# Kernel optimization log

Measured on AMD Instinct MI355X. Metric: run time of the kernel, lower is better.

The kernel has to match this reference:

```python
import jax, jax.numpy as jnp
import numpy as np

B, T, S, D, H, F = 8, 1024, 1024, 512, 8, 2048
LN_EPS = 1e-5


def _layernorm(x, g, b):
    m = jnp.mean(x, axis=-1, keepdims=True)
    v = jnp.mean((x - m) ** 2, axis=-1, keepdims=True)
    return (x - m) / jnp.sqrt(v + LN_EPS) * g + b


def setup_inputs() -> dict:
    key = jax.random.key(0)
    ks = jax.random.split(key, 32)
    p = lambda k, shape: jax.random.normal(k, shape, jnp.float32) * 0.02
    causal = jnp.where(jnp.triu(jnp.ones((T, T), dtype=bool), 1), -1e9, 0.0).astype(jnp.float32)
    return {
        "x": jax.random.normal(ks[0], (B, T, D), jnp.float32),
        "src_padding_mask": jnp.zeros((B, S, 1), jnp.float32),
        "src_subsq_mask": jnp.zeros((S, S), jnp.float32),  # unused by DecoderLayer math
        "tgt_padding_mask": jnp.zeros((B, T, 1), jnp.float32),
        "tgt_subsq_mask": causal,
        "mem_keys": jax.random.normal(ks[1], (B, S, D), jnp.float32),
        "mem_values": jax.random.normal(ks[2], (B, S, D), jnp.float32),
        # self-attention per-head params, stacked over heads (each head is full-D)
        "Wq_self": p(ks[3], (H, D, D)), "bq_self": p(ks[4], (H, D)),
        "Wk_self": p(ks[5], (H, D, D)), "bk_self": p(ks[6], (H, D)),
        "Wv_self": p(ks[7], (H, D, D)), "bv_self": p(ks[8], (H, D)),
        "Wo_self": p(ks[9], (H * D, D)), "bo_self": p(ks[10], (D,)),
        # memory (cross) attention: only Q per head; keys/values come from encoder
        "Wq_mem": p(ks[11], (H, D, D)), "bq_mem": p(ks[12], (H, D)),
        "Wo_mem": p(ks[13], (H * D, D)), "bo_mem": p(ks[14], (D,)),
        # FFN
        "W1": p(ks[15], (D, F)), "b1": p(ks[16], (F,)),
        "W2": p(ks[17], (F, D)), "b2": p(ks[18], (D,)),
        # LayerNorms
        "ln1_g": jnp.ones((D,), jnp.float32), "ln1_b": jnp.zeros((D,), jnp.float32),
        "ln2_g": jnp.ones((D,), jnp.float32), "ln2_b": jnp.zeros((D,), jnp.float32),
        "ln3_g": jnp.ones((D,), jnp.float32), "ln3_b": jnp.zeros((D,), jnp.float32),
    }


def reference(x, src_padding_mask, src_subsq_mask, tgt_padding_mask, tgt_subsq_mask,
              mem_keys, mem_values,
              Wq_self, bq_self, Wk_self, bk_self, Wv_self, bv_self, Wo_self, bo_self,
              Wq_mem, bq_mem, Wo_mem, bo_mem,
              W1, b1, W2, b2,
              ln1_g, ln1_b, ln2_g, ln2_b, ln3_g, ln3_b):
    b, t, d = x.shape
    h = Wq_self.shape[0]
    inv_sqrt_d = 1.0 / (d ** 0.5)

    # ---- multi-head self-attention (each head full d_model) ----
    q = jnp.einsum('btd,hde->bhte', x, Wq_self) + bq_self[None, :, None, :]
    k = jnp.einsum('btd,hde->bhte', x, Wk_self) + bk_self[None, :, None, :]
    v = jnp.einsum('btd,hde->bhte', x, Wv_self) + bv_self[None, :, None, :]
    att = jnp.einsum('bhte,bhse->bhts', q, k) * inv_sqrt_d
    att = att + tgt_padding_mask.transpose(0, 2, 1)[:, None, :, :]  # [B,1,1,T]
    att = att + tgt_subsq_mask[None, None, :, :]                     # [1,1,T,T]
    a = jax.nn.softmax(att, axis=-1)
    ho = jnp.einsum('bhts,bhse->bhte', a, v)
    cat = ho.transpose(0, 2, 1, 3).reshape(b, t, h * d)  # matches torch.cat head order
    sa = cat @ Wo_self + bo_self
    x1 = _layernorm(sa + x, ln1_g, ln1_b)  # dropout is identity at eval

    # ---- multi-head memory (cross) attention; keys/values shared across heads ----
    qm = jnp.einsum('btd,hde->bhte', x1, Wq_mem) + bq_mem[None, :, None, :]
    attm = jnp.einsum('bhte,bse->bhts', qm, mem_keys) * inv_sqrt_d
    attm = attm + src_padding_mask.transpose(0, 2, 1)[:, None, :, :]
    am = jax.nn.softmax(attm, axis=-1)
    hom = jnp.einsum('bhts,bse->bhte', am, mem_values)
    catm = hom.transpose(0, 2, 1, 3).reshape(b, t, h * d)
    ma = catm @ Wo_mem + bo_mem
    x2 = _layernorm(ma + x1, ln2_g, ln2_b)

    # ---- FFN ----
    ff = jax.nn.relu(x2 @ W1 + b1) @ W2 + b2
    out = _layernorm(ff + x2, ln3_g, ln3_b)
    return out
```

## Files before the change

### kernel.cpp

```cpp
#include <hip/hip_runtime.h>
#include <hip/hip_bf16.h>
#include <cstdint>

#define DEV __device__ __forceinline__

typedef __bf16 bf16_t;
typedef bf16_t bf16x8 __attribute__((ext_vector_type(8)));
typedef float  f32x4  __attribute__((ext_vector_type(4)));

static constexpr int B_ = 8, T_ = 1024, S_ = 1024, D_ = 512, H_ = 8, F_ = 2048;

typedef const __attribute__((address_space(1))) void* gas_ptr;
typedef __attribute__((address_space(3))) void* las_ptr;

DEV void gload_lds16(const void* g, void* l) {
  __builtin_amdgcn_global_load_lds((gas_ptr)g, (las_ptr)l, 16, 0, 0);
}

template<typename OutT, int EPI, int MI>
__global__ __launch_bounds__(256, (MI == 2) ? 3 : 2) void gemm_bt(
    const bf16_t* __restrict__ A,  int64_t aH, int64_t aB, int lda,
    const bf16_t* __restrict__ BT, int64_t bH, int64_t bB, int ldb,
    OutT* __restrict__ C,          int64_t cH, int64_t cB, int ldo,
    int K, int ZB,
    const float* __restrict__ bias, int64_t biasH, int64_t biasB,
    float scale,
    const float* __restrict__ pad, int64_t padB,
    const float* __restrict__ subsq, int subsq_ld, int causal,
    int initC, int kcap)
{
  constexpr int BM = MI * 32;

  const unsigned gx = gridDim.x, gy = gridDim.y;
  const unsigned nwg = gx * gy * gridDim.z;
  const unsigned orig = (blockIdx.z * gy + blockIdx.y) * gx + blockIdx.x;
  const unsigned q8 = nwg >> 3, r8 = nwg & 7;
  const unsigned xcd = orig & 7, cidx = orig >> 3;
  const unsigned swz = (xcd < r8 ? xcd * (q8 + 1)
                                 : r8 * (q8 + 1) + (xcd - r8) * q8) + cidx;
  const unsigned bz = swz / (gx * gy);
  const unsigned rm = swz - bz * gx * gy;
  const unsigned by = rm / gx;
  const unsigned bx = rm - by * gx;

  const int z  = bz;
  const int zh = z / ZB, zb = z - zh * ZB;
  A  += zh * aH + zb * aB;
  BT += zh * bH + zb * bB;
  C  += zh * cH + zb * cB;
  const int m0 = by * BM;
  const int n0 = bx << 7;

  __shared__ __align__(16) bf16_t As[2][BM * 64];
  __shared__ __align__(16) bf16_t Bs[2][128 * 64];

  const int tid  = threadIdx.x;
  const int lane = tid & 63;
  const int wr   = tid >> 7;
  const int wc   = (tid >> 6) & 1;

  f32x4 acc[MI][4] = {};

  const bool skip = (EPI == 2) && causal && (n0 >= m0 + BM);

  int Klim = K;
  if (kcap) { const int lim = m0 + BM; Klim = lim < K ? lim : K; }

  auto stage = [&](int buf, int kb) {
    #pragma unroll
    for (int i = 0; i < MI; ++i) {
      const int c = i * 256 + tid;
      const int row = c >> 3;
      const int col = (((c & 7) ^ (row & 7)) << 3);
      gload_lds16(A + (int64_t)(m0 + row) * lda + kb + col, &As[buf][c * 8]);
    }
    #pragma unroll
    for (int i = 0; i < 4; ++i) {
      const int c = i * 256 + tid;
      const int row = c >> 3;
      const int col = (((c & 7) ^ (row & 7)) << 3);
      gload_lds16(BT + (int64_t)(n0 + row) * ldb + kb + col, &Bs[buf][c * 8]);
    }
  };

  if (!skip) {
    const int NT = Klim >> 6;
    stage(0, 0);
    if (NT > 1) stage(1, 64);
    const int hi = lane >> 4, r7 = lane & 7;
    for (int t = 0; t < NT; ++t) {
      if (t + 1 < NT) {
        if constexpr (MI == 2) asm volatile("s_waitcnt vmcnt(6)" ::: "memory");
        else                   asm volatile("s_waitcnt vmcnt(8)" ::: "memory");
      } else {
        asm volatile("s_waitcnt vmcnt(0)" ::: "memory");
      }
      __builtin_amdgcn_s_barrier();
      __builtin_amdgcn_sched_barrier(0);
      const int cur = t & 1;
      bf16x8 af[MI][2], bq[4][2];
      #pragma unroll
      for (int ks = 0; ks < 2; ++ks) {
        #pragma unroll
        for (int i = 0; i < MI; ++i)
          af[i][ks] = *(const bf16x8*)&As[cur][(wr * (MI * 16) + i * 16 + (lane & 15)) * 64 + (((ks * 4 + hi) ^ r7) << 3)];
        #pragma unroll
        for (int i = 0; i < 4; ++i)
          bq[i][ks] = *(const bf16x8*)&Bs[cur][(wc * 64 + i * 16 + (lane & 15)) * 64 + (((ks * 4 + hi) ^ r7) << 3)];
      }
      asm volatile("s_waitcnt lgkmcnt(0)" ::: "memory");
      __builtin_amdgcn_sched_barrier(0);
      __builtin_amdgcn_s_barrier();
      if (t + 2 < NT) stage(cur, (t + 2) << 6);
      __builtin_amdgcn_sched_barrier(0);
      __builtin_amdgcn_s_setprio(1);
      #pragma unroll
      for (int ks = 0; ks < 2; ++ks)
        #pragma unroll
        for (int mi = 0; mi < MI; ++mi)
          #pragma unroll
          for (int ni = 0; ni < 4; ++ni)
            acc[mi][ni] = __builtin_amdgcn_mfma_f32_16x16x32_bf16(af[mi][ks], bq[ni][ks], acc[mi][ni], 0, 0, 0);
      __builtin_amdgcn_s_setprio(0);
    }
  }

  const float* bz_ = (EPI != 2 && bias) ? bias + zh * biasH + zb * biasB : nullptr;
  const float* pz  = (EPI == 2 && pad)  ? pad + zb * padB : nullptr;
  #pragma unroll
  for (int ni = 0; ni < 4; ++ni) {
    const int col = n0 + wc * 64 + ni * 16 + (lane & 15);
    const float badd = bz_ ? bz_[col] : 0.f;
    const float pv   = pz ? pz[col] : 0.f;
    #pragma unroll
    for (int mi = 0; mi < MI; ++mi) {
      const int rowb = m0 + wr * (MI * 16) + mi * 16 + ((lane >> 4) << 2);
      #pragma unroll
      for (int r = 0; r < 4; ++r) {
        const int row = rowb + r;
        const int64_t idx = (int64_t)row * ldo + col;
        float v = acc[mi][ni][r];
        if (EPI == 2) {
          if (skip) v = -1e9f;
          else {
            v = v * scale + pv;
            if (subsq) v += subsq[(int64_t)row * subsq_ld + col];
          }
        } else if (EPI == 3) {
          v += initC ? badd : (float)C[idx];
        } else {
          v += badd;
          if (EPI == 1) v = fmaxf(v, 0.f);
        }
        if constexpr (sizeof(OutT) == 2) C[idx] = (OutT)v;
        else                             C[idx] = v;
      }
    }
  }
}

__global__ __launch_bounds__(256) void softmax1024b(bf16_t* __restrict__ P)
{
  const int64_t row = blockIdx.x;
  const int tid = threadIdx.x;
  union { bf16_t b[4]; uint2 u; } in;
  in.u = ((const uint2*)(P + row * 1024))[tid];
  const float v0 = (float)in.b[0], v1 = (float)in.b[1];
  const float v2 = (float)in.b[2], v3 = (float)in.b[3];
  float m = fmaxf(fmaxf(v0, v1), fmaxf(v2, v3));
  #pragma unroll
  for (int off = 32; off; off >>= 1) m = fmaxf(m, __shfl_xor(m, off));
  __shared__ float red[8];
  if ((tid & 63) == 0) red[tid >> 6] = m;
  __syncthreads();
  m = fmaxf(fmaxf(red[0], red[1]), fmaxf(red[2], red[3]));
  const float e0 = __expf(v0 - m), e1 = __expf(v1 - m);
  const float e2 = __expf(v2 - m), e3 = __expf(v3 - m);
  float s = e0 + e1 + e2 + e3;
  #pragma unroll
  for (int off = 32; off; off >>= 1) s += __shfl_xor(s, off);
  if ((tid & 63) == 0) red[4 + (tid >> 6)] = s;
  __syncthreads();
  const float inv = 1.f / (red[4] + red[5] + red[6] + red[7]);
  union { bf16_t b[4]; uint2 u; } o;
  o.b[0] = (bf16_t)(e0 * inv); o.b[1] = (bf16_t)(e1 * inv);
  o.b[2] = (bf16_t)(e2 * inv); o.b[3] = (bf16_t)(e3 * inv);
  ((uint2*)(P + row * 1024))[tid] = o.u;
}

__global__ __launch_bounds__(128) void add_ln512(
    const float* __restrict__ a, const float* __restrict__ r,
    const float* __restrict__ g, const float* __restrict__ be,
    float* __restrict__ yf, bf16_t* __restrict__ yb)
{
  const int64_t row = blockIdx.x;
  const int tid = threadIdx.x;
  const float4 va = ((const float4*)(a + row * 512))[tid];
  const float4 vr = ((const float4*)(r + row * 512))[tid];
  const float x0 = va.x + vr.x, x1 = va.y + vr.y, x2 = va.z + vr.z, x3 = va.w + vr.w;
  float s = x0 + x1 + x2 + x3;
  float q = x0 * x0 + x1 * x1 + x2 * x2 + x3 * x3;
  #pragma unroll
  for (int off = 32; off; off >>= 1) { s += __shfl_xor(s, off); q += __shfl_xor(q, off); }
  __shared__ float red[4];
  if ((tid & 63) == 0) { red[tid >> 6] = s; red[2 + (tid >> 6)] = q; }
  __syncthreads();
  s = red[0] + red[1]; q = red[2] + red[3];
  const float mean = s * (1.f / 512.f);
  const float var  = q * (1.f / 512.f) - mean * mean;
  const float rstd = rsqrtf(var + 1e-5f);
  const float4 g4 = ((const float4*)g)[tid];
  const float4 b4 = ((const float4*)be)[tid];
  const float y0 = (x0 - mean) * rstd * g4.x + b4.x;
  const float y1 = (x1 - mean) * rstd * g4.y + b4.y;
  const float y2 = (x2 - mean) * rstd * g4.z + b4.z;
  const float y3 = (x3 - mean) * rstd * g4.w + b4.w;
  float4 o; o.x = y0; o.y = y1; o.z = y2; o.w = y3;
  ((float4*)(yf + row * 512))[tid] = o;
  if (yb) {
    union { bf16_t b[4]; uint2 u; } ob;
    ob.b[0] = (bf16_t)y0; ob.b[1] = (bf16_t)y1; ob.b[2] = (bf16_t)y2; ob.b[3] = (bf16_t)y3;
    ((uint2*)(yb + row * 512))[tid] = ob.u;
  }
}

template<typename InT>
__global__ __launch_bounds__(256) void tcast(
    const InT* __restrict__ src, bf16_t* __restrict__ dst, int R, int C)
{
  __shared__ float t[32][33];
  const int64_t zo = (int64_t)blockIdx.z * R * C;
  const int c0 = blockIdx.x << 5, r0 = blockIdx.y << 5;
  const int tx = threadIdx.x & 31, ty = threadIdx.x >> 5;
  #pragma unroll
  for (int i = 0; i < 32; i += 8)
    t[ty + i][tx] = (float)src[zo + (int64_t)(r0 + ty + i) * C + c0 + tx];
  __syncthreads();
  #pragma unroll
  for (int i = 0; i < 32; i += 8)
    dst[zo + (int64_t)(c0 + ty + i) * R + r0 + tx] = (bf16_t)t[tx][ty + i];
}

__global__ __launch_bounds__(256) void castf2b(
    const float* __restrict__ s, bf16_t* __restrict__ d, int n4)
{
  const int i = blockIdx.x * 256 + threadIdx.x;
  if (i >= n4) return;
  const float4 v = ((const float4*)s)[i];
  union { bf16_t b[4]; uint2 u; } o;
  o.b[0] = (bf16_t)v.x; o.b[1] = (bf16_t)v.y; o.b[2] = (bf16_t)v.z; o.b[3] = (bf16_t)v.w;
  ((uint2*)d)[i] = o.u;
}

__global__ __launch_bounds__(256) void pack3(
    const float* __restrict__ a, const float* __restrict__ b,
    const float* __restrict__ c, float* __restrict__ d, int n)
{
  const int i = blockIdx.x * 256 + threadIdx.x;
  if (i < n) { d[i] = a[i]; d[n + i] = b[i]; d[2 * n + i] = c[i]; }
}

extern "C" void kernel_launch(void* const* d_in, const int* in_sizes, int n_in,
                              void* d_out, int out_size, void* d_ws, size_t ws_size,
                              hipStream_t stream)
{
  const float* x       = (const float*)d_in[0];
  const float* src_pad = (const float*)d_in[1];
  const float* tgt_pad = (const float*)d_in[3];
  const float* tgt_sub = (const float*)d_in[4];
  const float* mk      = (const float*)d_in[5];
  const float* mv      = (const float*)d_in[6];
  const float* Wq  = (const float*)d_in[7];
  const float* bq  = (const float*)d_in[8];
  const float* Wk  = (const float*)d_in[9];
  const float* bk  = (const float*)d_in[10];
  const float* Wv  = (const float*)d_in[11];
  const float* bv  = (const float*)d_in[12];
  const float* Wo  = (const float*)d_in[13];
  const float* bo  = (const float*)d_in[14];
  const float* Wqm = (const float*)d_in[15];
  const float* bqm = (const float*)d_in[16];
  const float* Wom = (const float*)d_in[17];
  const float* bom = (const float*)d_in[18];
  const float* W1  = (const float*)d_in[19];
  const float* b1  = (const float*)d_in[20];
  const float* W2  = (const float*)d_in[21];
  const float* b2  = (const float*)d_in[22];
  const float* g1  = (const float*)d_in[23];
  const float* be1 = (const float*)d_in[24];
  const float* g2  = (const float*)d_in[25];
  const float* be2 = (const float*)d_in[26];
  const float* g3  = (const float*)d_in[27];
  const float* be3 = (const float*)d_in[28];
  float* outf = (float*)d_out;

  constexpr int64_t BTD = (int64_t)B_ * T_ * D_;
  constexpr int64_t BTS = (int64_t)B_ * T_ * S_;
  constexpr int64_t DD  = (int64_t)D_ * D_;
  const int M8 = B_ * T_;

  char* p = (char*)d_ws;
  auto alloc = [&](int64_t bytes) -> void* {
    char* r = p; p += (bytes + 255) & ~(int64_t)255; return (void*)r;
  };
  bf16_t* WTqkv = (bf16_t*)alloc(3 * H_ * DD * 2);
  bf16_t* WoT   = (bf16_t*)alloc((int64_t)D_ * H_ * D_ * 2);
  bf16_t* WqmT  = (bf16_t*)alloc(H_ * DD * 2);
  bf16_t* WomT  = (bf16_t*)alloc((int64_t)D_ * H_ * D_ * 2);
  bf16_t* W1T   = (bf16_t*)alloc((int64_t)F_ * D_ * 2);
  bf16_t* W2T   = (bf16_t*)alloc((int64_t)D_ * F_ * 2);
  float*  bqkv  = (float*)alloc(3 * H_ * D_ * 4);
  bf16_t* actb  = (bf16_t*)alloc(BTD * 2);
  bf16_t* mkb   = (bf16_t*)alloc(BTD * 2);
  bf16_t* mvT   = (bf16_t*)alloc(BTD * 2);
  float*  x1f   = (float*)alloc(BTD * 4);

  const int64_t remain = (int64_t)ws_size - (int64_t)(p - (char*)d_ws);
  const int64_t perG   = 3 * BTD * 2 + BTD * 2 + BTS * 2;
  const int64_t hoCat  = (int64_t)B_ * T_ * H_ * D_ * 2;
  int G = 0;
  for (int g = 8; g >= 1; g >>= 1)
    if (remain >= hoCat + (int64_t)g * perG + (4 << 20)) { G = g; break; }
  const int64_t needB = 3 * BTD * 2 + BTD * 2 + BTS * 2 + BTD * 2 + (1 << 20);
  if (G == 0 && remain < needB) return;

  const float scale = 1.0f / sqrtf((float)D_);
  dim3 blk(256);

  castf2b<<<dim3((unsigned)(BTD / 4 / 256)), blk, 0, stream>>>(x, actb, (int)(BTD / 4));
  castf2b<<<dim3((unsigned)(BTD / 4 / 256)), blk, 0, stream>>>(mk, mkb, (int)(BTD / 4));
  tcast<float><<<dim3(D_ / 32, S_ / 32, B_), blk, 0, stream>>>(mv, mvT, S_, D_);
  tcast<float><<<dim3(D_ / 32, D_ / 32, H_), blk, 0, stream>>>(Wq, WTqkv, D_, D_);
  tcast<float><<<dim3(D_ / 32, D_ / 32, H_), blk, 0, stream>>>(Wk, WTqkv + H_ * DD, D_, D_);
  tcast<float><<<dim3(D_ / 32, D_ / 32, H_), blk, 0, stream>>>(Wv, WTqkv + 2 * H_ * DD, D_, D_);
  tcast<float><<<dim3(D_ / 32, (H_ * D_) / 32, 1), blk, 0, stream>>>(Wo, WoT, H_ * D_, D_);
  tcast<float><<<dim3(D_ / 32, D_ / 32, H_), blk, 0, stream>>>(Wqm, WqmT, D_, D_);
  tcast<float><<<dim3(D_ / 32, (H_ * D_) / 32, 1), blk, 0, stream>>>(Wom, WomT, H_ * D_, D_);
  tcast<float><<<dim3(F_ / 32, D_ / 32, 1), blk, 0, stream>>>(W1, W1T, D_, F_);
  tcast<float><<<dim3(D_ / 32, F_ / 32, 1), blk, 0, stream>>>(W2, W2T, F_, D_);
  pack3<<<dim3((H_ * D_ + 255) / 256), blk, 0, stream>>>(bq, bk, bv, bqkv, H_ * D_);

  bf16_t* ffh = nullptr;

  if (G > 0) {
    bf16_t* hoAll = (bf16_t*)alloc(hoCat);
    bf16_t* qkv   = (bf16_t*)alloc(3 * G * BTD * 2);
    bf16_t* vt    = (bf16_t*)alloc((int64_t)G * BTD * 2);
    bf16_t* logit = (bf16_t*)alloc((int64_t)G * BTS * 2);
    ffh = qkv;

    for (int h0 = 0; h0 < H_; h0 += G) {
      gemm_bt<bf16_t, 0, 4><<<dim3(D_ / 128, M8 / 128, 3 * G), blk, 0, stream>>>(
          actb, 0, 0, D_,
          WTqkv + (int64_t)h0 * DD, (int64_t)H_ * DD, DD, D_,
          qkv, (int64_t)G * BTD, BTD, D_,
          D_, G,
          bqkv + h0 * D_, (int64_t)H_ * D_, D_,
          1.f, nullptr, 0, nullptr, 0, 0, 0, 0);
      tcast<bf16_t><<<dim3(D_ / 32, T_ / 32, G * B_), blk, 0, stream>>>(
          qkv + (int64_t)2 * G * BTD, vt, T_, D_);
      gemm_bt<bf16_t, 2, 4><<<dim3(S_ / 128, T_ / 128, G * B_), blk, 0, stream>>>(
          qkv, BTD, (int64_t)T_ * D_, D_,
          qkv + (int64_t)G * BTD, BTD, (int64_t)T_ * D_, D_,
          logit, BTS, (int64_t)T_ * S_, S_,
          D_, B_,
          nullptr, 0, 0,
          scale, tgt_pad, T_, tgt_sub, S_, 1, 0, 0);
      softmax1024b<<<dim3((unsigned)(G * B_ * T_)), blk, 0, stream>>>(logit);
      gemm_bt<bf16_t, 0, 4><<<dim3(D_ / 128, T_ / 128, G * B_), blk, 0, stream>>>(
          logit, BTS, (int64_t)T_ * S_, S_,
          vt, (int64_t)B_ * D_ * T_, (int64_t)D_ * T_, T_,
          hoAll + (int64_t)h0 * D_, D_, (int64_t)T_ * H_ * D_, H_ * D_,
          S_, B_,
          nullptr, 0, 0, 1.f, nullptr, 0, nullptr, 0, 0, 0, 1);
    }
    gemm_bt<float, 0, 2><<<dim3(D_ / 128, M8 / 64, 1), blk, 0, stream>>>(
        hoAll, 0, 0, H_ * D_, WoT, 0, 0, H_ * D_, outf, 0, 0, D_,
        H_ * D_, 1, bo, 0, 0, 1.f, nullptr, 0, nullptr, 0, 0, 0, 0);
    add_ln512<<<dim3(M8), dim3(128), 0, stream>>>(outf, x, g1, be1, x1f, actb);

    for (int h0 = 0; h0 < H_; h0 += G) {
      gemm_bt<bf16_t, 0, 4><<<dim3(D_ / 128, M8 / 128, G), blk, 0, stream>>>(
          actb, 0, 0, D_,
          WqmT + (int64_t)h0 * DD, 0, DD, D_,
          qkv, 0, BTD, D_,
          D_, G,
          bqm + h0 * D_, 0, D_,
          1.f, nullptr, 0, nullptr, 0, 0, 0, 0);
      gemm_bt<bf16_t, 2, 4><<<dim3(S_ / 128, T_ / 128, G * B_), blk, 0, stream>>>(
          qkv, BTD, (int64_t)T_ * D_, D_,
          mkb, 0, (int64_t)S_ * D_, D_,
          logit, BTS, (int64_t)T_ * S_, S_,
          D_, B_,
          nullptr, 0, 0,
          scale, src_pad, S_, nullptr, 0, 0, 0, 0);
      softmax1024b<<<dim3((unsigned)(G * B_ * T_)), blk, 0, stream>>>(logit);
      gemm_bt<bf16_t, 0, 4><<<dim3(D_ / 128, T_ / 128, G * B_), blk, 0, stream>>>(
          logit, BTS, (int64_t)T_ * S_, S_,
          mvT, 0, (int64_t)D_ * S_, S_,
          hoAll + (int64_t)h0 * D_, D_, (int64_t)T_ * H_ * D_, H_ * D_,
          S_, B_,
          nullptr, 0, 0, 1.f, nullptr, 0, nullptr, 0, 0, 0, 0);
    }
    gemm_bt<float, 0, 2><<<dim3(D_ / 128, M8 / 64, 1), blk, 0, stream>>>(
        hoAll, 0, 0, H_ * D_, WomT, 0, 0, H_ * D_, outf, 0, 0, D_,
        H_ * D_, 1, bom, 0, 0, 1.f, nullptr, 0, nullptr, 0, 0, 0, 0);
    add_ln512<<<dim3(M8), dim3(128), 0, stream>>>(outf, x1f, g2, be2, x1f, actb);
  } else {
    bf16_t* qkvH  = (bf16_t*)alloc(3 * BTD * 2);
    bf16_t* vtH   = (bf16_t*)alloc(BTD * 2);
    bf16_t* logit = (bf16_t*)alloc(BTS * 2);
    bf16_t* hoH   = (bf16_t*)alloc(BTD * 2);
    ffh = qkvH;

    for (int h = 0; h < H_; ++h) {
      gemm_bt<bf16_t, 0, 4><<<dim3(D_ / 128, M8 / 128, 3), blk, 0, stream>>>(
          actb, 0, 0, D_,
          WTqkv + (int64_t)h * DD, (int64_t)H_ * DD, 0, D_,
          qkvH, BTD, 0, D_,
          D_, 1,
          bqkv + h * D_, (int64_t)H_ * D_, 0,
          1.f, nullptr, 0, nullptr, 0, 0, 0, 0);
      tcast<bf16_t><<<dim3(D_ / 32, T_ / 32, B_), blk, 0, stream>>>(
          qkvH + 2 * BTD, vtH, T_, D_);
      gemm_bt<bf16_t, 2, 4><<<dim3(S_ / 128, T_ / 128, B_), blk, 0, stream>>>(
          qkvH, 0, (int64_t)T_ * D_, D_,
          qkvH + BTD, 0, (int64_t)T_ * D_, D_,
          logit, 0, (int64_t)T_ * S_, S_,
          D_, B_,
          nullptr, 0, 0,
          scale, tgt_pad, T_, tgt_sub, S_, 1, 0, 0);
      softmax1024b<<<dim3((unsigned)(B_ * T_)), blk, 0, stream>>>(logit);
      gemm_bt<bf16_t, 0, 4><<<dim3(D_ / 128, T_ / 128, B_), blk, 0, stream>>>(
          logit, 0, (int64_t)T_ * S_, S_,
          vtH, 0, (int64_t)D_ * T_, T_,
          hoH, 0, (int64_t)T_ * D_, D_,
          S_, B_,
          nullptr, 0, 0, 1.f, nullptr, 0, nullptr, 0, 0, 0, 1);
      gemm_bt<float, 3, 2><<<dim3(D_ / 128, M8 / 64, 1), blk, 0, stream>>>(
          hoH, 0, 0, D_,
          WoT + (int64_t)h * D_, 0, 0, H_ * D_,
          outf, 0, 0, D_,
          D_, 1,
          bo, 0, 0, 1.f, nullptr, 0, nullptr, 0, 0, (h == 0) ? 1 : 0, 0);
    }
    add_ln512<<<dim3(M8), dim3(128), 0, stream>>>(outf, x, g1, be1, x1f, actb);

    for (int h = 0; h < H_; ++h) {
      gemm_bt<bf16_t, 0, 4><<<dim3(D_ / 128, M8 / 128, 1), blk, 0, stream>>>(
          actb, 0, 0, D_,
          WqmT + (int64_t)h * DD, 0, 0, D_,
          qkvH, 0, 0, D_,
          D_, 1,
          bqm + h * D_, 0, 0,
          1.f, nullptr, 0, nullptr, 0, 0, 0, 0);
      gemm_bt<bf16_t, 2, 4><<<dim3(S_ / 128, T_ / 128, B_), blk, 0, stream>>>(
          qkvH, 0, (int64_t)T_ * D_, D_,
          mkb, 0, (int64_t)S_ * D_, D_,
          logit, 0, (int64_t)T_ * S_, S_,
          D_, B_,
          nullptr, 0, 0,
          scale, src_pad, S_, nullptr, 0, 0, 0, 0);
      softmax1024b<<<dim3((unsigned)(B_ * T_)), blk, 0, stream>>>(logit);
      gemm_bt<bf16_t, 0, 4><<<dim3(D_ / 128, T_ / 128, B_), blk, 0, stream>>>(
          logit, 0, (int64_t)T_ * S_, S_,
          mvT, 0, (int64_t)D_ * S_, S_,
          hoH, 0, (int64_t)T_ * D_, D_,
          S_, B_,
          nullptr, 0, 0, 1.f, nullptr, 0, nullptr, 0, 0, 0, 0);
      gemm_bt<float, 3, 2><<<dim3(D_ / 128, M8 / 64, 1), blk, 0, stream>>>(
          hoH, 0, 0, D_,
          WomT + (int64_t)h * D_, 0, 0, H_ * D_,
          outf, 0, 0, D_,
          D_, 1,
          bom, 0, 0, 1.f, nullptr, 0, nullptr, 0, 0, (h == 0) ? 1 : 0, 0);
    }
    add_ln512<<<dim3(M8), dim3(128), 0, stream>>>(outf, x1f, g2, be2, x1f, actb);
  }

  gemm_bt<bf16_t, 1, 4><<<dim3(F_ / 128, M8 / 128, 1), blk, 0, stream>>>(
      actb, 0, 0, D_, W1T, 0, 0, D_, ffh, 0, 0, F_,
      D_, 1, b1, 0, 0, 1.f, nullptr, 0, nullptr, 0, 0, 0, 0);
  gemm_bt<float, 0, 2><<<dim3(D_ / 128, M8 / 64, 1), blk, 0, stream>>>(
      ffh, 0, 0, F_, W2T, 0, 0, F_, outf, 0, 0, D_,
      F_, 1, b2, 0, 0, 1.f, nullptr, 0, nullptr, 0, 0, 0, 0);
  add_ln512<<<dim3(M8), dim3(128), 0, stream>>>(outf, x1f, g3, be3, outf, nullptr);

  (void)in_sizes; (void)n_in; (void)out_size;
}
```

Measured before the change: 1.147 ms.

## Skip masked causal tiles and use 64-row GEMM tiles throughout

Adds a causal mode in which fully masked logit tiles return early instead of writing -1e9. The softmax is templated so the causal variant reads and exponentiates only the valid prefix of each row, and writes only up to the next 64-column boundary. The PV GEMM's K cap then keeps unwritten entries out of the product. All bf16 GEMMs also switch from 128-row to 64-row tiles, raising block count and occupancy at the cost of less operand reuse per block.

```diff
diff --git a/kernel.cpp b/kernel.cpp
--- a/kernel.cpp
+++ b/kernel.cpp
@@ -51,6 +51,9 @@
   const int m0 = by * BM;
   const int n0 = bx << 7;
 
+  const bool skip = (EPI == 2) && causal && (n0 >= m0 + BM);
+  if (skip && causal == 2) return;
+
   __shared__ __align__(16) bf16_t As[2][BM * 64];
   __shared__ __align__(16) bf16_t Bs[2][128 * 64];
 
@@ -60,8 +63,6 @@
   const int wc   = (tid >> 6) & 1;
 
   f32x4 acc[MI][4] = {};
-
-  const bool skip = (EPI == 2) && causal && (n0 >= m0 + BM);
 
   int Klim = K;
   if (kcap) { const int lim = m0 + BM; Klim = lim < K ? lim : K; }
@@ -159,14 +160,22 @@
   }
 }
 
+template<int CAUSAL>
 __global__ __launch_bounds__(256) void softmax1024b(bf16_t* __restrict__ P)
 {
   const int64_t row = blockIdx.x;
+  const int len = CAUSAL ? (int)(row % T_) + 1 : 1024;
   const int tid = threadIdx.x;
-  union { bf16_t b[4]; uint2 u; } in;
-  in.u = ((const uint2*)(P + row * 1024))[tid];
-  const float v0 = (float)in.b[0], v1 = (float)in.b[1];
-  const float v2 = (float)in.b[2], v3 = (float)in.b[3];
+  const int j4 = tid << 2;
+  float v0 = -3e38f, v1 = -3e38f, v2 = -3e38f, v3 = -3e38f;
+  if (j4 < len) {
+    union { bf16_t b[4]; uint2 u; } in;
+    in.u = ((const uint2*)(P + row * 1024))[tid];
+    v0 = (float)in.b[0];
+    if (j4 + 1 < len) v1 = (float)in.b[1];
+    if (j4 + 2 < len) v2 = (float)in.b[2];
+    if (j4 + 3 < len) v3 = (float)in.b[3];
+  }
   float m = fmaxf(fmaxf(v0, v1), fmaxf(v2, v3));
   #pragma unroll
   for (int off = 32; off; off >>= 1) m = fmaxf(m, __shfl_xor(m, off));
@@ -174,18 +183,23 @@
   if ((tid & 63) == 0) red[tid >> 6] = m;
   __syncthreads();
   m = fmaxf(fmaxf(red[0], red[1]), fmaxf(red[2], red[3]));
-  const float e0 = __expf(v0 - m), e1 = __expf(v1 - m);
-  const float e2 = __expf(v2 - m), e3 = __expf(v3 - m);
+  const float e0 = (j4     < len) ? __expf(v0 - m) : 0.f;
+  const float e1 = (j4 + 1 < len) ? __expf(v1 - m) : 0.f;
+  const float e2 = (j4 + 2 < len) ? __expf(v2 - m) : 0.f;
+  const float e3 = (j4 + 3 < len) ? __expf(v3 - m) : 0.f;
   float s = e0 + e1 + e2 + e3;
   #pragma unroll
   for (int off = 32; off; off >>= 1) s += __shfl_xor(s, off);
   if ((tid & 63) == 0) red[4 + (tid >> 6)] = s;
   __syncthreads();
   const float inv = 1.f / (red[4] + red[5] + red[6] + red[7]);
-  union { bf16_t b[4]; uint2 u; } o;
-  o.b[0] = (bf16_t)(e0 * inv); o.b[1] = (bf16_t)(e1 * inv);
-  o.b[2] = (bf16_t)(e2 * inv); o.b[3] = (bf16_t)(e3 * inv);
-  ((uint2*)(P + row * 1024))[tid] = o.u;
+  const int lenc = CAUSAL ? ((len + 63) & ~63) : 1024;
+  if (j4 < lenc) {
+    union { bf16_t b[4]; uint2 u; } o;
+    o.b[0] = (bf16_t)(e0 * inv); o.b[1] = (bf16_t)(e1 * inv);
+    o.b[2] = (bf16_t)(e2 * inv); o.b[3] = (bf16_t)(e3 * inv);
+    ((uint2*)(P + row * 1024))[tid] = o.u;
+  }
 }
 
 __global__ __launch_bounds__(128) void add_ln512(
@@ -350,7 +364,7 @@
     ffh = qkv;
 
     for (int h0 = 0; h0 < H_; h0 += G) {
-      gemm_bt<bf16_t, 0, 4><<<dim3(D_ / 128, M8 / 128, 3 * G), blk, 0, stream>>>(
+      gemm_bt<bf16_t, 0, 2><<<dim3(D_ / 128, M8 / 64, 3 * G), blk, 0, stream>>>(
           actb, 0, 0, D_,
           WTqkv + (int64_t)h0 * DD, (int64_t)H_ * DD, DD, D_,
           qkv, (int64_t)G * BTD, BTD, D_,
@@ -359,15 +373,15 @@
           1.f, nullptr, 0, nullptr, 0, 0, 0, 0);
       tcast<bf16_t><<<dim3(D_ / 32, T_ / 32, G * B_), blk, 0, stream>>>(
           qkv + (int64_t)2 * G * BTD, vt, T_, D_);
-      gemm_bt<bf16_t, 2, 4><<<dim3(S_ / 128, T_ / 128, G * B_), blk, 0, stream>>>(
+      gemm_bt<bf16_t, 2, 2><<<dim3(S_ / 128, T_ / 64, G * B_), blk, 0, stream>>>(
           qkv, BTD, (int64_t)T_ * D_, D_,
           qkv + (int64_t)G * BTD, BTD, (int64_t)T_ * D_, D_,
           logit, BTS, (int64_t)T_ * S_, S_,
           D_, B_,
           nullptr, 0, 0,
-          scale, tgt_pad, T_, tgt_sub, S_, 1, 0, 0);
-      softmax1024b<<<dim3((unsigned)(G * B_ * T_)), blk, 0, stream>>>(logit);
-      gemm_bt<bf16_t, 0, 4><<<dim3(D_ / 128, T_ / 128, G * B_), blk, 0, stream>>>(
+          scale, tgt_pad, T_, tgt_sub, S_, 2, 0, 0);
+      softmax1024b<1><<<dim3((unsigned)(G * B_ * T_)), blk, 0, stream>>>(logit);
+      gemm_bt<bf16_t, 0, 2><<<dim3(D_ / 128, T_ / 64, G * B_), blk, 0, stream>>>(
           logit, BTS, (int64_t)T_ * S_, S_,
           vt, (int64_t)B_ * D_ * T_, (int64_t)D_ * T_, T_,
           hoAll + (int64_t)h0 * D_, D_, (int64_t)T_ * H_ * D_, H_ * D_,
@@ -380,22 +394,22 @@
     add_ln512<<<dim3(M8), dim3(128), 0, stream>>>(outf, x, g1, be1, x1f, actb);
 
     for (int h0 = 0; h0 < H_; h0 += G) {
-      gemm_bt<bf16_t, 0, 4><<<dim3(D_ / 128, M8 / 128, G), blk, 0, stream>>>(
+      gemm_bt<bf16_t, 0, 2><<<dim3(D_ / 128, M8 / 64, G), blk, 0, stream>>>(
           actb, 0, 0, D_,
           WqmT + (int64_t)h0 * DD, 0, DD, D_,
           qkv, 0, BTD, D_,
           D_, G,
           bqm + h0 * D_, 0, D_,
           1.f, nullptr, 0, nullptr, 0, 0, 0, 0);
-      gemm_bt<bf16_t, 2, 4><<<dim3(S_ / 128, T_ / 128, G * B_), blk, 0, stream>>>(
+      gemm_bt<bf16_t, 2, 2><<<dim3(S_ / 128, T_ / 64, G * B_), blk, 0, stream>>>(
           qkv, BTD, (int64_t)T_ * D_, D_,
           mkb, 0, (int64_t)S_ * D_, D_,
           logit, BTS, (int64_t)T_ * S_, S_,
           D_, B_,
           nullptr, 0, 0,
           scale, src_pad, S_, nullptr, 0, 0, 0, 0);
-      softmax1024b<<<dim3((unsigned)(G * B_ * T_)), blk, 0, stream>>>(logit);
-      gemm_bt<bf16_t, 0, 4><<<dim3(D_ / 128, T_ / 128, G * B_), blk, 0, stream>>>(
+      softmax1024b<0><<<dim3((unsigned)(G * B_ * T_)), blk, 0, stream>>>(logit);
+      gemm_bt<bf16_t, 0, 2><<<dim3(D_ / 128, T_ / 64, G * B_), blk, 0, stream>>>(
           logit, BTS, (int64_t)T_ * S_, S_,
           mvT, 0, (int64_t)D_ * S_, S_,
           hoAll + (int64_t)h0 * D_, D_, (int64_t)T_ * H_ * D_, H_ * D_,
@@ -414,7 +428,7 @@
     ffh = qkvH;
 
     for (int h = 0; h < H_; ++h) {
-      gemm_bt<bf16_t, 0, 4><<<dim3(D_ / 128, M8 / 128, 3), blk, 0, stream>>>(
+      gemm_bt<bf16_t, 0, 2><<<dim3(D_ / 128, M8 / 64, 3), blk, 0, stream>>>(
           actb, 0, 0, D_,
           WTqkv + (int64_t)h * DD, (int64_t)H_ * DD, 0, D_,
           qkvH, BTD, 0, D_,
@@ -423,15 +437,15 @@
           1.f, nullptr, 0, nullptr, 0, 0, 0, 0);
       tcast<bf16_t><<<dim3(D_ / 32, T_ / 32, B_), blk, 0, stream>>>(
           qkvH + 2 * BTD, vtH, T_, D_);
-      gemm_bt<bf16_t, 2, 4><<<dim3(S_ / 128, T_ / 128, B_), blk, 0, stream>>>(
+      gemm_bt<bf16_t, 2, 2><<<dim3(S_ / 128, T_ / 64, B_), blk, 0, stream>>>(
           qkvH, 0, (int64_t)T_ * D_, D_,
           qkvH + BTD, 0, (int64_t)T_ * D_, D_,
           logit, 0, (int64_t)T_ * S_, S_,
           D_, B_,
           nullptr, 0, 0,
-          scale, tgt_pad, T_, tgt_sub, S_, 1, 0, 0);
-      softmax1024b<<<dim3((unsigned)(B_ * T_)), blk, 0, stream>>>(logit);
-      gemm_bt<bf16_t, 0, 4><<<dim3(D_ / 128, T_ / 128, B_), blk, 0, stream>>>(
+          scale, tgt_pad, T_, tgt_sub, S_, 2, 0, 0);
+      softmax1024b<1><<<dim3((unsigned)(B_ * T_)), blk, 0, stream>>>(logit);
+      gemm_bt<bf16_t, 0, 2><<<dim3(D_ / 128, T_ / 64, B_), blk, 0, stream>>>(
           logit, 0, (int64_t)T_ * S_, S_,
           vtH, 0, (int64_t)D_ * T_, T_,
           hoH, 0, (int64_t)T_ * D_, D_,
@@ -447,22 +461,22 @@
     add_ln512<<<dim3(M8), dim3(128), 0, stream>>>(outf, x, g1, be1, x1f, actb);
 
     for (int h = 0; h < H_; ++h) {
-      gemm_bt<bf16_t, 0, 4><<<dim3(D_ / 128, M8 / 128, 1), blk, 0, stream>>>(
+      gemm_bt<bf16_t, 0, 2><<<dim3(D_ / 128, M8 / 64, 1), blk, 0, stream>>>(
           actb, 0, 0, D_,
           WqmT + (int64_t)h * DD, 0, 0, D_,
           qkvH, 0, 0, D_,
           D_, 1,
           bqm + h * D_, 0, 0,
           1.f, nullptr, 0, nullptr, 0, 0, 0, 0);
-      gemm_bt<bf16_t, 2, 4><<<dim3(S_ / 128, T_ / 128, B_), blk, 0, stream>>>(
+      gemm_bt<bf16_t, 2, 2><<<dim3(S_ / 128, T_ / 64, B_), blk, 0, stream>>>(
           qkvH, 0, (int64_t)T_ * D_, D_,
           mkb, 0, (int64_t)S_ * D_, D_,
           logit, 0, (int64_t)T_ * S_, S_,
           D_, B_,
           nullptr, 0, 0,
           scale, src_pad, S_, nullptr, 0, 0, 0, 0);
-      softmax1024b<<<dim3((unsigned)(B_ * T_)), blk, 0, stream>>>(logit);
-      gemm_bt<bf16_t, 0, 4><<<dim3(D_ / 128, T_ / 128, B_), blk, 0, stream>>>(
+      softmax1024b<0><<<dim3((unsigned)(B_ * T_)), blk, 0, stream>>>(logit);
+      gemm_bt<bf16_t, 0, 2><<<dim3(D_ / 128, T_ / 64, B_), blk, 0, stream>>>(
           logit, 0, (int64_t)T_ * S_, S_,
           mvT, 0, (int64_t)D_ * S_, S_,
           hoH, 0, (int64_t)T_ * D_, D_,
@@ -478,7 +492,7 @@
     add_ln512<<<dim3(M8), dim3(128), 0, stream>>>(outf, x1f, g2, be2, x1f, actb);
   }
 
-  gemm_bt<bf16_t, 1, 4><<<dim3(F_ / 128, M8 / 128, 1), blk, 0, stream>>>(
+  gemm_bt<bf16_t, 1, 2><<<dim3(F_ / 128, M8 / 64, 1), blk, 0, stream>>>(
       actb, 0, 0, D_, W1T, 0, 0, D_, ffh, 0, 0, F_,
       D_, 1, b1, 0, 0, 1.f, nullptr, 0, nullptr, 0, 0, 0, 0);
   gemm_bt<float, 0, 2><<<dim3(D_ / 128, M8 / 64, 1), blk, 0, stream>>>(
```

Result: no change. 1.130 ms (-1.5%).
